# Kernel tuning notes

Hardware: AMD Instinct MI355X
Metric: run time of the kernel (lower is better)

The kernel has to match this reference:

```python
import jax, jax.numpy as jnp
import numpy as np

B, S, H, NH, L, ML = 4, 2048, 768, 8, 128, 15
DH = H // NH
PERIOD = 16  # newline every 16 tokens -> 15 content tokens per line


def _layernorm(x, g, b, eps=1e-5):
    m = x.mean(-1, keepdims=True)
    v = ((x - m) ** 2).mean(-1, keepdims=True)
    return (x - m) / jnp.sqrt(v + eps) * g + b


def setup_inputs() -> dict:
    key = jax.random.key(0)
    ks = jax.random.split(key, 8)
    sc = 0.02
    return {
        "hidden": jax.random.normal(ks[0], (B, S, H), jnp.float32),
        "in_proj_w": jax.random.normal(ks[1], (3 * H, H), jnp.float32) * sc,
        "in_proj_b": jnp.zeros((3 * H,), jnp.float32),
        "out_proj_w": jax.random.normal(ks[2], (H, H), jnp.float32) * sc,
        "out_proj_b": jnp.zeros((H,), jnp.float32),
        "W1": jax.random.normal(ks[3], (H, 2 * H), jnp.float32) * sc,
        "b1": jnp.zeros((H,), jnp.float32),
        "g1": jnp.ones((H,), jnp.float32),
        "be1": jnp.zeros((H,), jnp.float32),
        "W2": jax.random.normal(ks[4], (H, H), jnp.float32) * sc,
        "b2": jnp.zeros((H,), jnp.float32),
        "g2": jnp.ones((H,), jnp.float32),
        "be2": jnp.zeros((H,), jnp.float32),
        "W3": jax.random.normal(ks[5], (1, H), jnp.float32) * sc,
        "b3": jnp.zeros((1,), jnp.float32),
        # padded ragged line structure (what the torch loops derive from newline positions)
        "line_starts": jnp.tile(jnp.arange(L, dtype=jnp.int32) * PERIOD, (B, 1)),  # [B,L]
        "line_lens": jnp.full((B, L), ML, jnp.int32),                              # [B,L]
        "context_len": jnp.full((B,), S, jnp.int32),                               # [B]
    }


def reference(hidden, in_proj_w, in_proj_b, out_proj_w, out_proj_b,
              W1, b1, g1, be1, W2, b2, g2, be2, W3, b3,
              line_starts, line_lens, context_len):
    # --- gather per-line tokens into a padded [B, L, ML, H] block ---
    pos = line_starts[:, :, None] + jnp.arange(ML, dtype=line_starts.dtype)      # [B,L,ML]
    tok_mask = jnp.arange(ML)[None, None, :] < line_lens[:, :, None]             # [B,L,ML]
    pos_c = jnp.clip(pos, 0, S - 1)
    bidx = jnp.arange(B)[:, None, None]
    line_tok = hidden[bidx, pos_c]                                               # [B,L,ML,H]

    # --- nn.MultiheadAttention: query=line tokens, key/value=global context ---
    Wq, Wk, Wv = jnp.split(in_proj_w, 3, axis=0)
    bq, bk, bv = jnp.split(in_proj_b, 3, axis=0)
    q = (line_tok @ Wq.T + bq).reshape(B, L, ML, NH, DH)
    k = (hidden @ Wk.T + bk).reshape(B, S, NH, DH)
    v = (hidden @ Wv.T + bv).reshape(B, S, NH, DH)

    scale = 1.0 / np.float32(np.sqrt(DH))
    scores = jnp.einsum('blmhd,bshd->blhms', q, k) * scale                       # [B,L,NH,ML,S]
    kmask = jnp.arange(S)[None, :] < context_len[:, None]                        # [B,S]
    scores = jnp.where(kmask[:, None, None, None, :], scores, -1e9)
    attn = jax.nn.softmax(scores, axis=-1)
    o = jnp.einsum('blhms,bshd->blmhd', attn, v).reshape(B, L, ML, H)
    o = o @ out_proj_w.T + out_proj_b                                            # [B,L,ML,H]

    # --- masked mean-pool over the line's tokens ---
    m = tok_mask[..., None].astype(hidden.dtype)
    denom = jnp.maximum(line_lens, 1)[..., None].astype(hidden.dtype)            # [B,L,1]
    line_mean = (line_tok * m).sum(2) / denom                                    # [B,L,H]
    attn_mean = (o * m).sum(2) / denom                                           # [B,L,H]

    # --- classifier: Linear -> LN -> GELU -> Residual(Linear->LN->GELU) -> Linear ---
    x = jnp.concatenate([line_mean, attn_mean], axis=-1)                         # [B,L,2H]
    x = jax.nn.gelu(_layernorm(x @ W1.T + b1, g1, be1), approximate=False)
    x = x + jax.nn.gelu(_layernorm(x @ W2.T + b2, g2, be2), approximate=False)
    logits = (x @ W3.T + b3)[..., 0]                                             # [B,L]

    # empty lines get logit -10 (as in the torch loop)
    logits = jnp.where(line_lens > 0, logits, jnp.asarray(-10.0, logits.dtype))
    return jax.nn.sigmoid(logits)
```

## Files before the change

kernel.cpp:

```cpp
#include <hip/hip_runtime.h>
#include <hip/hip_bf16.h>
#include <cmath>

using bf16 = __hip_bfloat16;
typedef __attribute__((ext_vector_type(8))) short short8;
typedef __attribute__((ext_vector_type(4))) short s16x4;
typedef __attribute__((ext_vector_type(4))) float f32x4;

#define B_   4
#define S_   2048
#define H_   768
#define H2_  1536
#define H3_  2304
#define NH_  8
#define DH_  96
#define L_   128
#define ML_  15
#define LG_  8
#define QR_  128
#define CH_  32
#define NS_  2
#define SLC_ (S_ / NS_)
#define ELD  36
#define VTLD 40
#define KLD  104
#define VTR  112
#define ALD  40

__device__ __forceinline__ float gelu_exact(float v) {
    return 0.5f * v * (1.0f + erff(v * 0.7071067811865475f));
}
__device__ __forceinline__ short f2bs(float f) {
    bf16 h = __float2bfloat16(f);
    return *reinterpret_cast<short*>(&h);
}
__device__ __forceinline__ short8 ld_frag8(const short* p) {
    union { short8 v; s16x4 h[2]; } u;
    u.h[0] = *(const s16x4*)p;
    u.h[1] = *(const s16x4*)(p + 4);
    return u.v;
}

__global__ __launch_bounds__(256) void f2b2_k(
    const float* __restrict__ s1, bf16* __restrict__ d1, int n1,
    const float* __restrict__ s2, bf16* __restrict__ d2, int n2)
{
    const int i = (blockIdx.x * 256 + threadIdx.x) * 8;
    const float* src; bf16* dst; int off;
    if (i < n1) { src = s1; dst = d1; off = i; }
    else if (i < n1 + n2) { src = s2; dst = d2; off = i - n1; }
    else return;
    float4 a = *(const float4*)(src + off);
    float4 b = *(const float4*)(src + off + 4);
    short8 r;
    r[0] = f2bs(a.x); r[1] = f2bs(a.y); r[2] = f2bs(a.z); r[3] = f2bs(a.w);
    r[4] = f2bs(b.x); r[5] = f2bs(b.y); r[6] = f2bs(b.z); r[7] = f2bs(b.w);
    *(short8*)(dst + off) = r;
}

template <typename T>
__device__ __forceinline__ void stage8(const T* src, bf16* dst);
template <>
__device__ __forceinline__ void stage8<bf16>(const bf16* src, bf16* dst) {
    *(int4*)dst = *(const int4*)src;
}
template <>
__device__ __forceinline__ void stage8<float>(const float* src, bf16* dst) {
    float4 a = *(const float4*)src;
    float4 b = *(const float4*)(src + 4);
    short8 r;
    r[0] = f2bs(a.x); r[1] = f2bs(a.y); r[2] = f2bs(a.z); r[3] = f2bs(a.w);
    r[4] = f2bs(b.x); r[5] = f2bs(b.y); r[6] = f2bs(b.z); r[7] = f2bs(b.w);
    *(short8*)dst = r;
}

__global__ __launch_bounds__(256) void gemm128_qkv(
    const bf16* __restrict__ A, const bf16* __restrict__ Bm,
    const float* __restrict__ bias, bf16* __restrict__ qk,
    bf16* __restrict__ vt, int M, int K)
{
    __shared__ alignas(16) bf16 As[128 * ALD];
    __shared__ alignas(16) bf16 Bs[128 * ALD];
    const int t = threadIdx.x;
    const int wave = t >> 6, lane = t & 63;
    const int l15 = lane & 15, quad = lane >> 4;
    const int m0 = blockIdx.x * 128, n0 = blockIdx.y * 128;
    const int wm = wave & 1, wn = wave >> 1;
    const int srow = t >> 1, scol = (t & 1) * 16;

    const bf16* aP = A + (size_t)(m0 + srow) * K + scol;
    const bf16* bP = Bm + (size_t)(n0 + srow) * K + scol;
    bf16* aL = &As[srow * ALD + scol];
    bf16* bL = &Bs[srow * ALD + scol];

    f32x4 acc[4][4];
#pragma unroll
    for (int i = 0; i < 4; i++)
#pragma unroll
        for (int j = 0; j < 4; j++) acc[i][j] = (f32x4){0.f, 0.f, 0.f, 0.f};

    for (int k0 = 0; k0 < K; k0 += 32) {
        int4 ra0 = *(const int4*)(aP + k0);
        int4 ra1 = *(const int4*)(aP + k0 + 8);
        int4 rb0 = *(const int4*)(bP + k0);
        int4 rb1 = *(const int4*)(bP + k0 + 8);
        __syncthreads();
        *(int4*)aL = ra0; *(int4*)(aL + 8) = ra1;
        *(int4*)bL = rb0; *(int4*)(bL + 8) = rb1;
        __syncthreads();
        short8 af[4], bfq[4];
#pragma unroll
        for (int i = 0; i < 4; i++)
            af[i] = *(const short8*)&As[(wm * 64 + i * 16 + l15) * ALD + quad * 8];
#pragma unroll
        for (int j = 0; j < 4; j++)
            bfq[j] = *(const short8*)&Bs[(wn * 64 + j * 16 + l15) * ALD + quad * 8];
#pragma unroll
        for (int i = 0; i < 4; i++)
#pragma unroll
            for (int j = 0; j < 4; j++)
                acc[i][j] = __builtin_amdgcn_mfma_f32_16x16x32_bf16(af[i], bfq[j], acc[i][j], 0, 0, 0);
    }

    if (n0 < H2_) {
#pragma unroll
        for (int j = 0; j < 4; j++) {
            const int col = n0 + wn * 64 + j * 16 + l15;
            const float bv = bias[col];
#pragma unroll
            for (int i = 0; i < 4; i++) {
                const int row = m0 + wm * 64 + i * 16 + quad * 4;
#pragma unroll
                for (int r = 0; r < 4; r++)
                    qk[(size_t)(row + r) * H2_ + col] = __float2bfloat16(acc[i][j][r] + bv);
            }
        }
    } else {
#pragma unroll
        for (int j = 0; j < 4; j++) {
            const int col = n0 + wn * 64 + j * 16 + l15;
            const float bv = bias[col];
            const int dfull = col - H2_;
            const int hh = dfull / DH_, d = dfull - hh * DH_;
#pragma unroll
            for (int i = 0; i < 4; i++) {
                const int row = m0 + wm * 64 + i * 16 + quad * 4;
                const int b = row >> 11, s = row & (S_ - 1);
                s16x4 pk;
#pragma unroll
                for (int r = 0; r < 4; r++) pk[r] = f2bs(acc[i][j][r] + bv);
                *(s16x4*)&vt[((size_t)(b * NH_ + hh) * DH_ + d) * S_ + s] = pk;
            }
        }
    }
}

template <typename TA, typename TB, bool OUT_BF16>
__global__ __launch_bounds__(256) void gemm_bt(
    const TA* __restrict__ A, const TB* __restrict__ Bm,
    const float* __restrict__ bias, void* __restrict__ Cout,
    int M, int N, int K, int ldc, int coff)
{
    __shared__ alignas(16) bf16 As[64 * ALD];
    __shared__ alignas(16) bf16 Bs[64 * ALD];
    const int t = threadIdx.x;
    const int wave = t >> 6, lane = t & 63;
    const int l15 = lane & 15, quad = lane >> 4;
    const int m0 = blockIdx.x * 64, n0 = blockIdx.y * 64;
    const int srow = t >> 2, schk = (t & 3) * 8;

    const TA* aPtr = A + (size_t)(m0 + srow) * K + schk;
    const TB* bPtr = Bm + (size_t)(n0 + srow) * K + schk;

    f32x4 acc[4] = {{0.f,0.f,0.f,0.f},{0.f,0.f,0.f,0.f},
                    {0.f,0.f,0.f,0.f},{0.f,0.f,0.f,0.f}};
    const int aoff = (wave * 16 + l15) * ALD + quad * 8;

    for (int k0 = 0; k0 < K; k0 += 32) {
        __syncthreads();
        stage8<TA>(aPtr + k0, &As[srow * ALD + schk]);
        stage8<TB>(bPtr + k0, &Bs[srow * ALD + schk]);
        __syncthreads();
        short8 af = *(const short8*)&As[aoff];
#pragma unroll
        for (int nt = 0; nt < 4; nt++) {
            short8 bfr = *(const short8*)&Bs[(nt * 16 + l15) * ALD + quad * 8];
            acc[nt] = __builtin_amdgcn_mfma_f32_16x16x32_bf16(af, bfr, acc[nt], 0, 0, 0);
        }
    }

#pragma unroll
    for (int nt = 0; nt < 4; nt++) {
        int col = n0 + nt * 16 + l15;
        float bv = bias[col];
#pragma unroll
        for (int r = 0; r < 4; r++) {
            int row = m0 + wave * 16 + quad * 4 + r;
            float v = acc[nt][r] + bv;
            if (OUT_BF16) ((bf16*)Cout)[(size_t)row * ldc + coff + col] = __float2bfloat16(v);
            else          ((float*)Cout)[(size_t)row * ldc + coff + col] = v;
        }
    }
}

__global__ __launch_bounds__(256) void attn_slice(
    const bf16* __restrict__ qk, const bf16* __restrict__ vtg,
    const int* __restrict__ line_starts, const int* __restrict__ line_lens,
    const int* __restrict__ context_len,
    bf16* __restrict__ Opart, float* __restrict__ Dpart)
{
    __shared__ alignas(16) union {
        short Qs[QR_ * KLD];
        struct {
            short Ks[CH_ * KLD];
            short Vt[VTR * VTLD];
            short Es[QR_ * ELD];
        } s;
    } U;

    const int t = threadIdx.x;
    const int idx = blockIdx.x;
    const int slice = blockIdx.y;
    const int lg = idx & 15;
    const int bh = idx >> 4;
    const int h = bh & 7, b = bh >> 3;
    const int ctx = context_len[b];
    const int wave = t >> 6, lane = t & 63;
    const int l15 = lane & 15, quad = lane >> 4;

    for (int ii = t; ii < QR_ * 12; ii += 256) {
        const int r = ii / 12, ck = ii - r * 12;
        int4 val; val.x = val.y = val.z = val.w = 0;
        if (r < LG_ * ML_) {
            const int li = r / ML_, m = r - li * ML_;
            const int line = lg * LG_ + li;
            const int len = line_lens[b * L_ + line];
            if (m < len) {
                int sPos = line_starts[b * L_ + line] + m;
                sPos = min(max(sPos, 0), S_ - 1);
                val = *(const int4*)(qk + (size_t)(b * S_ + sPos) * H2_ + h * DH_ + ck * 8);
            }
        }
        *(int4*)&U.Qs[r * KLD + ck * 8] = val;
    }
    __syncthreads();

    short8 qf[2][3];
#pragma unroll
    for (int st = 0; st < 2; st++)
#pragma unroll
        for (int kf = 0; kf < 3; kf++)
            qf[st][kf] = *(const short8*)(U.Qs + ((wave + 4 * st) * 16 + l15) * KLD + kf * 32 + quad * 8);
    __syncthreads();

    f32x4 Oacc[2][7];
#pragma unroll
    for (int st = 0; st < 2; st++)
#pragma unroll
        for (int nt = 0; nt < 7; nt++) Oacc[st][nt] = (f32x4){0.f, 0.f, 0.f, 0.f};

    const float scale = 0.10206207261596577f;
    const size_t kbase = (size_t)b * S_ * H2_ + H_ + h * DH_;
    const size_t vbase = (size_t)(b * NH_ + h) * DH_ * S_;
    const int cbase = slice * SLC_;

    const int k0r = t / 12,        k0c = t - k0r * 12;
    const int k1r = (256 + t) / 12, k1c = (256 + t) - k1r * 12;
    const int v0d = t >> 2,        v0s = (t & 3) * 8;
    const int v1d = (256 + t) >> 2, v1s = ((256 + t) & 3) * 8;
    const int on_r = t >> 4, on_c = t & 15;

    int4 rk0, rk1, rv0, rv1;
    {
        rk0 = *(const int4*)(qk + kbase + (size_t)(cbase + k0r) * H2_ + k0c * 8);
        rv0 = *(const int4*)(vtg + vbase + (size_t)v0d * S_ + cbase + v0s);
        if (t < 128) {
            rk1 = *(const int4*)(qk + kbase + (size_t)(cbase + k1r) * H2_ + k1c * 8);
            rv1 = *(const int4*)(vtg + vbase + (size_t)v1d * S_ + cbase + v1s);
        }
    }

    for (int ci = 0; ci < SLC_ / CH_; ci++) {
        const int c0 = cbase + ci * CH_;
        __syncthreads();
        *(int4*)&U.s.Ks[k0r * KLD + k0c * 8] = rk0;
        *(int4*)&U.s.Vt[v0d * VTLD + v0s] = rv0;
        if (t < 128) {
            *(int4*)&U.s.Ks[k1r * KLD + k1c * 8] = rk1;
            *(int4*)&U.s.Vt[v1d * VTLD + v1s] = rv1;
        }
        {
            unsigned int lo = (c0 + 2 * on_c)     < ctx ? 0x3f80u : 0u;
            unsigned int hi = (c0 + 2 * on_c + 1) < ctx ? 0x3f80u : 0u;
            ((unsigned int*)&U.s.Vt[(96 + on_r) * VTLD])[on_c] = lo | (hi << 16);
        }
        __syncthreads();

        if (ci + 1 < SLC_ / CH_) {
            const int cn = c0 + CH_;
            rk0 = *(const int4*)(qk + kbase + (size_t)(cn + k0r) * H2_ + k0c * 8);
            rv0 = *(const int4*)(vtg + vbase + (size_t)v0d * S_ + cn + v0s);
            if (t < 128) {
                rk1 = *(const int4*)(qk + kbase + (size_t)(cn + k1r) * H2_ + k1c * 8);
                rv1 = *(const int4*)(vtg + vbase + (size_t)v1d * S_ + cn + v1s);
            }
        }

        f32x4 acc[2][2] = {{{0.f,0.f,0.f,0.f},{0.f,0.f,0.f,0.f}},
                           {{0.f,0.f,0.f,0.f},{0.f,0.f,0.f,0.f}}};
#pragma unroll
        for (int ns = 0; ns < 2; ns++)
#pragma unroll
            for (int kf = 0; kf < 3; kf++) {
                short8 kfr = *(const short8*)(U.s.Ks + (ns * 16 + l15) * KLD + kf * 32 + quad * 8);
                acc[0][ns] = __builtin_amdgcn_mfma_f32_16x16x32_bf16(kfr, qf[0][kf], acc[0][ns], 0, 0, 0);
                acc[1][ns] = __builtin_amdgcn_mfma_f32_16x16x32_bf16(kfr, qf[1][kf], acc[1][ns], 0, 0, 0);
            }

#pragma unroll
        for (int st = 0; st < 2; st++)
#pragma unroll
            for (int ns = 0; ns < 2; ns++) {
                s16x4 wv;
#pragma unroll
                for (int r = 0; r < 4; r++) {
                    const int s = c0 + ns * 16 + quad * 4 + r;
                    float e = (s < ctx) ? __expf(acc[st][ns][r] * scale) : 0.f;
                    wv[r] = f2bs(e);
                }
                *(s16x4*)&U.s.Es[((wave + 4 * st) * 16 + l15) * ELD + ns * 16 + quad * 4] = wv;
            }

        short8 pf0 = ld_frag8(U.s.Es + (wave * 16 + l15) * ELD + quad * 8);
        short8 pf1 = ld_frag8(U.s.Es + ((wave + 4) * 16 + l15) * ELD + quad * 8);
#pragma unroll
        for (int nt = 0; nt < 7; nt++) {
            short8 vfr = *(const short8*)&U.s.Vt[(nt * 16 + l15) * VTLD + quad * 8];
            Oacc[0][nt] = __builtin_amdgcn_mfma_f32_16x16x32_bf16(pf0, vfr, Oacc[0][nt], 0, 0, 0);
            Oacc[1][nt] = __builtin_amdgcn_mfma_f32_16x16x32_bf16(pf1, vfr, Oacc[1][nt], 0, 0, 0);
        }
    }

    const size_t pb = (size_t)(slice * 512 + idx) * QR_;
#pragma unroll
    for (int st = 0; st < 2; st++)
#pragma unroll
        for (int r = 0; r < 4; r++) {
            const int row = (wave + 4 * st) * 16 + quad * 4 + r;
#pragma unroll
            for (int nt = 0; nt < 6; nt++)
                Opart[(pb + row) * DH_ + nt * 16 + l15] = __float2bfloat16(Oacc[st][nt][r]);
            if (l15 == 0) Dpart[pb + row] = Oacc[st][6][r];
        }
}

__global__ __launch_bounds__(256) void combine_pool(
    const bf16* __restrict__ Opart, const float* __restrict__ Dpart,
    const int* __restrict__ line_lens, bf16* __restrict__ opool)
{
    __shared__ float invd[LG_ * ML_];
    __shared__ int lens_s[LG_];
    const int idx = blockIdx.x;
    const int lg = idx & 15, bh = idx >> 4;
    const int h = bh & 7, b = bh >> 3;
    const int t = threadIdx.x;
    if (t < LG_) lens_s[t] = line_lens[b * L_ + lg * LG_ + t];
    if (t < LG_ * ML_) {
        float ds = 0.f;
#pragma unroll
        for (int s = 0; s < NS_; s++)
            ds += Dpart[(size_t)(s * 512 + idx) * QR_ + t];
        invd[t] = ds > 0.f ? 1.f / ds : 0.f;
    }
    __syncthreads();
    for (int q = t; q < LG_ * DH_; q += 256) {
        const int li = q / DH_, d = q - li * DH_;
        const int mm = min(lens_s[li], ML_);
        float acc = 0.f;
        for (int m = 0; m < mm; m++) {
            const int row = li * ML_ + m;
            float o = 0.f;
#pragma unroll
            for (int s = 0; s < NS_; s++)
                o += __bfloat162float(Opart[((size_t)(s * 512 + idx) * QR_ + row) * DH_ + d]);
            acc += o * invd[row];
        }
        const int line = lg * LG_ + li;
        opool[(size_t)(b * L_ + line) * H_ + h * DH_ + d] =
            __float2bfloat16(acc / (float)max(lens_s[li], 1));
    }
}

__global__ __launch_bounds__(256) void line_mean_k(
    const bf16* __restrict__ hidden, const int* __restrict__ line_starts,
    const int* __restrict__ line_lens, bf16* __restrict__ x)
{
    const int blk = blockIdx.x;
    const int b = blk >> 7, line = blk & 127;
    const int len = line_lens[b * L_ + line];
    const int start = line_starts[b * L_ + line];
    const int mm = min(len, ML_);
    const float inv = 1.f / (float)max(len, 1);
    for (int d = threadIdx.x; d < H_; d += 256) {
        float s = 0.f;
        for (int m = 0; m < mm; m++) {
            int sp = min(max(start + m, 0), S_ - 1);
            s += __bfloat162float(hidden[(size_t)(b * S_ + sp) * H_ + d]);
        }
        x[(size_t)blk * H2_ + d] = __float2bfloat16(s * inv);
    }
}

__global__ __launch_bounds__(256) void ln_gelu_k(
    const float* __restrict__ hin, const float* __restrict__ g,
    const float* __restrict__ be, float* __restrict__ uout, bf16* __restrict__ ubf)
{
    __shared__ float red[16];
    const int row = blockIdx.x, t = threadIdx.x;
    const float* hr = hin + (size_t)row * H_;
    float v[3];
    float s1 = 0.f, s2 = 0.f;
#pragma unroll
    for (int k = 0; k < 3; k++) {
        v[k] = hr[t + k * 256];
        s1 += v[k]; s2 += v[k] * v[k];
    }
#pragma unroll
    for (int m = 1; m < 64; m <<= 1) { s1 += __shfl_xor(s1, m, 64); s2 += __shfl_xor(s2, m, 64); }
    const int wave = t >> 6, lane = t & 63;
    if (lane == 0) { red[wave] = s1; red[8 + wave] = s2; }
    __syncthreads();
    s1 = red[0] + red[1] + red[2] + red[3];
    s2 = red[8] + red[9] + red[10] + red[11];
    const float mean = s1 * (1.f / H_);
    const float var = s2 * (1.f / H_) - mean * mean;
    const float rstd = 1.f / sqrtf(var + 1e-5f);
#pragma unroll
    for (int k = 0; k < 3; k++) {
        const int d = t + k * 256;
        float y = (v[k] - mean) * rstd * g[d] + be[d];
        y = gelu_exact(y);
        uout[(size_t)row * H_ + d] = y;
        ubf[(size_t)row * H_ + d] = __float2bfloat16(y);
    }
}

__global__ __launch_bounds__(256) void final_k(
    const float* __restrict__ h2, const float* __restrict__ u,
    const float* __restrict__ g2, const float* __restrict__ be2,
    const float* __restrict__ W3, const float* __restrict__ b3,
    const int* __restrict__ line_lens, float* __restrict__ out)
{
    __shared__ float red[16];
    const int row = blockIdx.x, t = threadIdx.x;
    const float* hr = h2 + (size_t)row * H_;
    float v[3];
    float s1 = 0.f, s2 = 0.f;
#pragma unroll
    for (int k = 0; k < 3; k++) {
        v[k] = hr[t + k * 256];
        s1 += v[k]; s2 += v[k] * v[k];
    }
#pragma unroll
    for (int m = 1; m < 64; m <<= 1) { s1 += __shfl_xor(s1, m, 64); s2 += __shfl_xor(s2, m, 64); }
    const int wave = t >> 6, lane = t & 63;
    if (lane == 0) { red[wave] = s1; red[8 + wave] = s2; }
    __syncthreads();
    s1 = red[0] + red[1] + red[2] + red[3];
    s2 = red[8] + red[9] + red[10] + red[11];
    const float mean = s1 * (1.f / H_);
    const float var = s2 * (1.f / H_) - mean * mean;
    const float rstd = 1.f / sqrtf(var + 1e-5f);
    float dotp = 0.f;
#pragma unroll
    for (int k = 0; k < 3; k++) {
        const int d = t + k * 256;
        float y = (v[k] - mean) * rstd * g2[d] + be2[d];
        y = u[(size_t)row * H_ + d] + gelu_exact(y);
        dotp += y * W3[d];
    }
#pragma unroll
    for (int m = 1; m < 64; m <<= 1) dotp += __shfl_xor(dotp, m, 64);
    __syncthreads();
    if (lane == 0) red[wave] = dotp;
    __syncthreads();
    if (t == 0) {
        float logit = red[0] + red[1] + red[2] + red[3] + b3[0];
        if (line_lens[row] <= 0) logit = -10.f;
        out[row] = 1.f / (1.f + __expf(-logit));
    }
}

extern "C" void kernel_launch(void* const* d_in, const int* in_sizes, int n_in,
                              void* d_out, int out_size, void* d_ws, size_t ws_size,
                              hipStream_t stream)
{
    const float* hidden     = (const float*)d_in[0];
    const float* in_proj_w  = (const float*)d_in[1];
    const float* in_proj_b  = (const float*)d_in[2];
    const float* out_proj_w = (const float*)d_in[3];
    const float* out_proj_b = (const float*)d_in[4];
    const float* W1         = (const float*)d_in[5];
    const float* b1         = (const float*)d_in[6];
    const float* g1         = (const float*)d_in[7];
    const float* be1        = (const float*)d_in[8];
    const float* W2         = (const float*)d_in[9];
    const float* b2         = (const float*)d_in[10];
    const float* g2         = (const float*)d_in[11];
    const float* be2        = (const float*)d_in[12];
    const float* W3         = (const float*)d_in[13];
    const float* b3         = (const float*)d_in[14];
    const int* line_starts  = (const int*)d_in[15];
    const int* line_lens    = (const int*)d_in[16];
    const int* context_len  = (const int*)d_in[17];

    const int BL = B_ * L_;
    const size_t nh = (size_t)B_ * S_ * H_;
    const size_t nw = (size_t)H3_ * H_;
    const size_t opart_n = (size_t)NS_ * 512 * QR_ * DH_;

    char* w = (char*)d_ws;
    bf16* qk    = (bf16*)w;  w += (size_t)B_ * S_ * H2_ * sizeof(bf16);
    bf16* vtg   = (bf16*)w;  w += (size_t)B_ * NH_ * DH_ * S_ * sizeof(bf16);
    char* ovl = w;
    bf16* hb    = (bf16*)ovl;
    bf16* wqkvb = (bf16*)(ovl + nh * sizeof(bf16));
    bf16* Opart = (bf16*)ovl;
    w = ovl + opart_n * sizeof(bf16);
    float* Dpart = (float*)w; w += (size_t)NS_ * 512 * QR_ * sizeof(float);
    bf16* opool = (bf16*)w;  w += (size_t)BL * H_ * sizeof(bf16);
    bf16* x     = (bf16*)w;  w += (size_t)BL * H2_ * sizeof(bf16);
    float* h1   = (float*)w; w += (size_t)BL * H_ * sizeof(float);
    float* uu   = (float*)w; w += (size_t)BL * H_ * sizeof(float);
    bf16* ubf   = (bf16*)w;  w += (size_t)BL * H_ * sizeof(bf16);
    float* h2   = (float*)w; w += (size_t)BL * H_ * sizeof(float);

    f2b2_k<<<(int)((nh + nw) / (256 * 8)), 256, 0, stream>>>(
        hidden, hb, (int)nh, in_proj_w, wqkvb, (int)nw);

    gemm128_qkv<<<dim3(B_ * S_ / 128, H3_ / 128), 256, 0, stream>>>(
        hb, wqkvb, in_proj_b, qk, vtg, B_ * S_, H_);
    line_mean_k<<<BL, 256, 0, stream>>>(hb, line_starts, line_lens, x);
    attn_slice<<<dim3(512, NS_), 256, 0, stream>>>(
        qk, vtg, line_starts, line_lens, context_len, Opart, Dpart);
    combine_pool<<<512, 256, 0, stream>>>(Opart, Dpart, line_lens, opool);
    gemm_bt<bf16, float, true><<<dim3(BL / 64, H_ / 64), 256, 0, stream>>>(
        opool, out_proj_w, out_proj_b, x, BL, H_, H_, H2_, H_);
    gemm_bt<bf16, float, false><<<dim3(BL / 64, H_ / 64), 256, 0, stream>>>(
        x, W1, b1, h1, BL, H_, H2_, H_, 0);
    ln_gelu_k<<<BL, 256, 0, stream>>>(h1, g1, be1, uu, ubf);
    gemm_bt<bf16, float, false><<<dim3(BL / 64, H_ / 64), 256, 0, stream>>>(
        ubf, W2, b2, h2, BL, H_, H_, H_, 0);
    final_k<<<BL, 256, 0, stream>>>(h2, uu, g2, be2, W3, b3, line_lens, (float*)d_out);
}
```

Before: 345.6 us.

## Prefetch GEMM tiles into registers, widen QKV k-step, skip mask work on full chunks

The QKV GEMM now stages 64-wide K tiles with a padded LDS stride and prefetches the next tile into registers while computing the current one. The generic GEMM gets the same register prefetch, so global loads overlap the MFMA work. The attention kernel stops rewriting the ones/mask row of Vt when the chunk state has not changed, and uses an unmasked exp path for chunks entirely inside the context. The trade-off is higher register use from the prefetch buffers and a larger LDS footprint in the QKV GEMM.

```diff
diff --git a/kernel.cpp b/kernel.cpp
--- a/kernel.cpp
+++ b/kernel.cpp
@@ -26,6 +26,7 @@
 #define KLD  104
 #define VTR  112
 #define ALD  40
+#define ALQ  72
 
 __device__ __forceinline__ float gelu_exact(float v) {
     return 0.5f * v * (1.0f + erff(v * 0.7071067811865475f));
@@ -58,19 +59,24 @@
     *(short8*)(dst + off) = r;
 }
 
-template <typename T>
-__device__ __forceinline__ void stage8(const T* src, bf16* dst);
-template <>
-__device__ __forceinline__ void stage8<bf16>(const bf16* src, bf16* dst) {
-    *(int4*)dst = *(const int4*)src;
-}
-template <>
-__device__ __forceinline__ void stage8<float>(const float* src, bf16* dst) {
-    float4 a = *(const float4*)src;
-    float4 b = *(const float4*)(src + 4);
+template <typename T> struct Pk8;
+template <> struct Pk8<bf16>  { int4 v; };
+template <> struct Pk8<float> { float4 a, b; };
+template <typename T> __device__ __forceinline__ Pk8<T> ld8(const T* p);
+template <> __device__ __forceinline__ Pk8<bf16> ld8(const bf16* p) {
+    Pk8<bf16> r; r.v = *(const int4*)p; return r;
+}
+template <> __device__ __forceinline__ Pk8<float> ld8(const float* p) {
+    Pk8<float> r; r.a = *(const float4*)p; r.b = *(const float4*)(p + 4); return r;
+}
+template <typename T> __device__ __forceinline__ void st8(const Pk8<T>& v, bf16* dst);
+template <> __device__ __forceinline__ void st8<bf16>(const Pk8<bf16>& v, bf16* dst) {
+    *(int4*)dst = v.v;
+}
+template <> __device__ __forceinline__ void st8<float>(const Pk8<float>& v, bf16* dst) {
     short8 r;
-    r[0] = f2bs(a.x); r[1] = f2bs(a.y); r[2] = f2bs(a.z); r[3] = f2bs(a.w);
-    r[4] = f2bs(b.x); r[5] = f2bs(b.y); r[6] = f2bs(b.z); r[7] = f2bs(b.w);
+    r[0] = f2bs(v.a.x); r[1] = f2bs(v.a.y); r[2] = f2bs(v.a.z); r[3] = f2bs(v.a.w);
+    r[4] = f2bs(v.b.x); r[5] = f2bs(v.b.y); r[6] = f2bs(v.b.z); r[7] = f2bs(v.b.w);
     *(short8*)dst = r;
 }
 
@@ -79,19 +85,19 @@
     const float* __restrict__ bias, bf16* __restrict__ qk,
     bf16* __restrict__ vt, int M, int K)
 {
-    __shared__ alignas(16) bf16 As[128 * ALD];
-    __shared__ alignas(16) bf16 Bs[128 * ALD];
+    __shared__ alignas(16) bf16 As[128 * ALQ];
+    __shared__ alignas(16) bf16 Bs[128 * ALQ];
     const int t = threadIdx.x;
     const int wave = t >> 6, lane = t & 63;
     const int l15 = lane & 15, quad = lane >> 4;
     const int m0 = blockIdx.x * 128, n0 = blockIdx.y * 128;
     const int wm = wave & 1, wn = wave >> 1;
-    const int srow = t >> 1, scol = (t & 1) * 16;
+    const int srow = t >> 1, scol = (t & 1) * 32;
 
     const bf16* aP = A + (size_t)(m0 + srow) * K + scol;
     const bf16* bP = Bm + (size_t)(n0 + srow) * K + scol;
-    bf16* aL = &As[srow * ALD + scol];
-    bf16* bL = &Bs[srow * ALD + scol];
+    bf16* aL = &As[srow * ALQ + scol];
+    bf16* bL = &Bs[srow * ALQ + scol];
 
     f32x4 acc[4][4];
 #pragma unroll
@@ -99,27 +105,43 @@
 #pragma unroll
         for (int j = 0; j < 4; j++) acc[i][j] = (f32x4){0.f, 0.f, 0.f, 0.f};
 
-    for (int k0 = 0; k0 < K; k0 += 32) {
-        int4 ra0 = *(const int4*)(aP + k0);
-        int4 ra1 = *(const int4*)(aP + k0 + 8);
-        int4 rb0 = *(const int4*)(bP + k0);
-        int4 rb1 = *(const int4*)(bP + k0 + 8);
+    int4 ra[4], rb[4];
+#pragma unroll
+    for (int c = 0; c < 4; c++) {
+        ra[c] = *(const int4*)(aP + c * 8);
+        rb[c] = *(const int4*)(bP + c * 8);
+    }
+
+    for (int k0 = 0; k0 < K; k0 += 64) {
         __syncthreads();
-        *(int4*)aL = ra0; *(int4*)(aL + 8) = ra1;
-        *(int4*)bL = rb0; *(int4*)(bL + 8) = rb1;
+#pragma unroll
+        for (int c = 0; c < 4; c++) {
+            *(int4*)(aL + c * 8) = ra[c];
+            *(int4*)(bL + c * 8) = rb[c];
+        }
         __syncthreads();
-        short8 af[4], bfq[4];
-#pragma unroll
-        for (int i = 0; i < 4; i++)
-            af[i] = *(const short8*)&As[(wm * 64 + i * 16 + l15) * ALD + quad * 8];
-#pragma unroll
-        for (int j = 0; j < 4; j++)
-            bfq[j] = *(const short8*)&Bs[(wn * 64 + j * 16 + l15) * ALD + quad * 8];
-#pragma unroll
-        for (int i = 0; i < 4; i++)
+        if (k0 + 64 < K) {
+#pragma unroll
+            for (int c = 0; c < 4; c++) {
+                ra[c] = *(const int4*)(aP + k0 + 64 + c * 8);
+                rb[c] = *(const int4*)(bP + k0 + 64 + c * 8);
+            }
+        }
+#pragma unroll
+        for (int kf = 0; kf < 2; kf++) {
+            short8 af[4], bfq[4];
+#pragma unroll
+            for (int i = 0; i < 4; i++)
+                af[i] = *(const short8*)&As[(wm * 64 + i * 16 + l15) * ALQ + kf * 32 + quad * 8];
 #pragma unroll
             for (int j = 0; j < 4; j++)
-                acc[i][j] = __builtin_amdgcn_mfma_f32_16x16x32_bf16(af[i], bfq[j], acc[i][j], 0, 0, 0);
+                bfq[j] = *(const short8*)&Bs[(wn * 64 + j * 16 + l15) * ALQ + kf * 32 + quad * 8];
+#pragma unroll
+            for (int i = 0; i < 4; i++)
+#pragma unroll
+                for (int j = 0; j < 4; j++)
+                    acc[i][j] = __builtin_amdgcn_mfma_f32_16x16x32_bf16(af[i], bfq[j], acc[i][j], 0, 0, 0);
+        }
     }
 
     if (n0 < H2_) {
@@ -171,16 +193,25 @@
 
     const TA* aPtr = A + (size_t)(m0 + srow) * K + schk;
     const TB* bPtr = Bm + (size_t)(n0 + srow) * K + schk;
+    bf16* aL = &As[srow * ALD + schk];
+    bf16* bL = &Bs[srow * ALD + schk];
 
     f32x4 acc[4] = {{0.f,0.f,0.f,0.f},{0.f,0.f,0.f,0.f},
                     {0.f,0.f,0.f,0.f},{0.f,0.f,0.f,0.f}};
     const int aoff = (wave * 16 + l15) * ALD + quad * 8;
 
+    Pk8<TA> pa = ld8<TA>(aPtr);
+    Pk8<TB> pb = ld8<TB>(bPtr);
+
     for (int k0 = 0; k0 < K; k0 += 32) {
         __syncthreads();
-        stage8<TA>(aPtr + k0, &As[srow * ALD + schk]);
-        stage8<TB>(bPtr + k0, &Bs[srow * ALD + schk]);
+        st8<TA>(pa, aL);
+        st8<TB>(pb, bL);
         __syncthreads();
+        if (k0 + 32 < K) {
+            pa = ld8<TA>(aPtr + k0 + 32);
+            pb = ld8<TB>(bPtr + k0 + 32);
+        }
         short8 af = *(const short8*)&As[aoff];
 #pragma unroll
         for (int nt = 0; nt < 4; nt++) {
@@ -280,6 +311,8 @@
         }
     }
 
+    int ones_state = -1;
+
     for (int ci = 0; ci < SLC_ / CH_; ci++) {
         const int c0 = cbase + ci * CH_;
         __syncthreads();
@@ -290,9 +323,13 @@
             *(int4*)&U.s.Vt[v1d * VTLD + v1s] = rv1;
         }
         {
-            unsigned int lo = (c0 + 2 * on_c)     < ctx ? 0x3f80u : 0u;
-            unsigned int hi = (c0 + 2 * on_c + 1) < ctx ? 0x3f80u : 0u;
-            ((unsigned int*)&U.s.Vt[(96 + on_r) * VTLD])[on_c] = lo | (hi << 16);
+            const int st_now = (c0 + CH_ <= ctx) ? 1 : ((c0 >= ctx) ? 0 : 2);
+            if (st_now != ones_state || st_now == 2) {
+                unsigned int lo = (c0 + 2 * on_c)     < ctx ? 0x3f80u : 0u;
+                unsigned int hi = (c0 + 2 * on_c + 1) < ctx ? 0x3f80u : 0u;
+                ((unsigned int*)&U.s.Vt[(96 + on_r) * VTLD])[on_c] = lo | (hi << 16);
+                ones_state = st_now;
+            }
         }
         __syncthreads();
 
@@ -317,19 +354,32 @@
                 acc[1][ns] = __builtin_amdgcn_mfma_f32_16x16x32_bf16(kfr, qf[1][kf], acc[1][ns], 0, 0, 0);
             }
 
-#pragma unroll
-        for (int st = 0; st < 2; st++)
-#pragma unroll
-            for (int ns = 0; ns < 2; ns++) {
-                s16x4 wv;
-#pragma unroll
-                for (int r = 0; r < 4; r++) {
-                    const int s = c0 + ns * 16 + quad * 4 + r;
-                    float e = (s < ctx) ? __expf(acc[st][ns][r] * scale) : 0.f;
-                    wv[r] = f2bs(e);
+        if (c0 + CH_ <= ctx) {
+#pragma unroll
+            for (int st = 0; st < 2; st++)
+#pragma unroll
+                for (int ns = 0; ns < 2; ns++) {
+                    s16x4 wv;
+#pragma unroll
+                    for (int r = 0; r < 4; r++)
+                        wv[r] = f2bs(__expf(acc[st][ns][r] * scale));
+                    *(s16x4*)&U.s.Es[((wave + 4 * st) * 16 + l15) * ELD + ns * 16 + quad * 4] = wv;
                 }
-                *(s16x4*)&U.s.Es[((wave + 4 * st) * 16 + l15) * ELD + ns * 16 + quad * 4] = wv;
-            }
+        } else {
+#pragma unroll
+            for (int st = 0; st < 2; st++)
+#pragma unroll
+                for (int ns = 0; ns < 2; ns++) {
+                    s16x4 wv;
+#pragma unroll
+                    for (int r = 0; r < 4; r++) {
+                        const int s = c0 + ns * 16 + quad * 4 + r;
+                        float e = (s < ctx) ? __expf(acc[st][ns][r] * scale) : 0.f;
+                        wv[r] = f2bs(e);
+                    }
+                    *(s16x4*)&U.s.Es[((wave + 4 * st) * 16 + l15) * ELD + ns * 16 + quad * 4] = wv;
+                }
+        }
 
         short8 pf0 = ld_frag8(U.s.Es + (wave * 16 + l15) * ELD + quad * 8);
         short8 pf1 = ld_frag8(U.s.Es + ((wave + 4) * 16 + l15) * ELD + quad * 8);
```

Result: slower. 440.6 us (+27.5%).
